# Kernel optimization log

Hardware: AMD Instinct MI355X
Metric: run time of the kernel (lower is better)

## Reference

```python
import jax, jax.numpy as jnp
import numpy as np

FP8_MAX = 448.0  # max representable magnitude of float8_e4m3fn


def _quantize_tensorwise(x):
    """Tensor-wise fp8 quantization. Returns (fp8 tensor, inverse_scale) where
    dequant = fp8.astype(f32) * inverse_scale (matches Fp8Quantization.quantize_tensorwise)."""
    amax = jnp.max(jnp.abs(x))
    inv_scale = jnp.maximum(amax / FP8_MAX, jnp.float32(1e-12))
    q = (x / inv_scale).astype(jnp.float8_e4m3fn)
    return q, inv_scale


def _fp8_mm(qa, qb, sa, sb):
    # scaled fp8 GEMM: accumulate in f32, apply product of per-tensor inverse scales
    return (qa.astype(jnp.float32) @ qb.astype(jnp.float32)) * (sa * sb)


def setup_inputs() -> dict:
    key = jax.random.key(0)
    k1, k2, k3 = jax.random.split(key, 3)
    x = jax.random.normal(k1, (4, 2048, 2048), dtype=jnp.float32)
    weight = jax.random.normal(k2, (2048, 2048), dtype=jnp.float32) * 0.02
    bias = jax.random.normal(k3, (2048,), dtype=jnp.float32) * 0.01
    return {"x": x, "weight": weight, "bias": bias}


def reference(x, weight, bias):
    # flatten leading dims: inputmat = input.view(-1, K)
    K = x.shape[-1]
    xm = x.reshape(-1, K)                      # [T, K]
    qx, sx = _quantize_tensorwise(xm)          # fp8 input + inverse scale
    qwt, swt = _quantize_tensorwise(weight.T)  # fp8 weight^T [K, N] + inverse scale
    out = _fp8_mm(qx, qwt, sx, swt) + bias     # [T, N]
    return out.reshape(*x.shape[:-1], -1)
```

## Files before the change

### kernel.cpp

```cpp
#include <hip/hip_runtime.h>
#include <stdint.h>

typedef float f32x4 __attribute__((ext_vector_type(4)));
typedef int   i32x4 __attribute__((ext_vector_type(4)));
typedef int   i32x8 __attribute__((ext_vector_type(8)));

__device__ __forceinline__ float amax4(float4 v) {
  return fmaxf(fmaxf(fabsf(v.x), fabsf(v.y)), fmaxf(fabsf(v.z), fabsf(v.w)));
}

__global__ __launch_bounds__(256) void amax2_kernel(
    const float* __restrict__ x, int nx4,
    const float* __restrict__ w, int nw4,
    int xblocks, int* __restrict__ out) {
  const float4* src;
  int n4, j0, stride, slot;
  if ((int)blockIdx.x < xblocks) {
    src = (const float4*)x; n4 = nx4; slot = 0;
    j0 = blockIdx.x * blockDim.x + threadIdx.x;
    stride = xblocks * blockDim.x;
  } else {
    src = (const float4*)w; n4 = nw4; slot = 1;
    j0 = (blockIdx.x - xblocks) * blockDim.x + threadIdx.x;
    stride = (gridDim.x - xblocks) * blockDim.x;
  }
  float m0 = 0.f, m1 = 0.f, m2 = 0.f, m3 = 0.f;
  int j = j0;
  for (; j + 3 * stride < n4; j += 4 * stride) {
    float4 v0 = src[j];
    float4 v1 = src[j + stride];
    float4 v2 = src[j + 2 * stride];
    float4 v3 = src[j + 3 * stride];
    m0 = fmaxf(m0, amax4(v0));
    m1 = fmaxf(m1, amax4(v1));
    m2 = fmaxf(m2, amax4(v2));
    m3 = fmaxf(m3, amax4(v3));
  }
  for (; j < n4; j += stride) m0 = fmaxf(m0, amax4(src[j]));
  float m = fmaxf(fmaxf(m0, m1), fmaxf(m2, m3));
#pragma unroll
  for (int off = 32; off; off >>= 1)
    m = fmaxf(m, __shfl_down(m, off, 64));
  __shared__ float red[4];
  const int lane = threadIdx.x & 63;
  const int wv = threadIdx.x >> 6;
  if (lane == 0) red[wv] = m;
  __syncthreads();
  if (threadIdx.x == 0) {
    m = fmaxf(fmaxf(red[0], red[1]), fmaxf(red[2], red[3]));
    atomicMax(out + slot, (int)__float_as_uint(m));
  }
}

__global__ __launch_bounds__(256) void quant2_kernel(
    const float* __restrict__ x, unsigned char* __restrict__ qx, int nx4,
    const float* __restrict__ w, unsigned char* __restrict__ qw, int nw4,
    int xblocks, const unsigned* __restrict__ amax2) {
  const float4* src;
  unsigned* dst;
  int n4, j0, stride;
  float amax;
  if ((int)blockIdx.x < xblocks) {
    src = (const float4*)x; dst = (unsigned*)qx; n4 = nx4;
    amax = __uint_as_float(amax2[0]);
    j0 = blockIdx.x * blockDim.x + threadIdx.x;
    stride = xblocks * blockDim.x;
  } else {
    src = (const float4*)w; dst = (unsigned*)qw; n4 = nw4;
    amax = __uint_as_float(amax2[1]);
    j0 = (blockIdx.x - xblocks) * blockDim.x + threadIdx.x;
    stride = (gridDim.x - xblocks) * blockDim.x;
  }
  const float inv_scale = fmaxf(amax / 448.0f, 1e-12f);
  int j = j0;
  for (; j + 3 * stride < n4; j += 4 * stride) {
    float4 v0 = src[j];
    float4 v1 = src[j + stride];
    float4 v2 = src[j + 2 * stride];
    float4 v3 = src[j + 3 * stride];
#pragma unroll
    for (int u = 0; u < 4; u++) {
      float4 v = (u == 0) ? v0 : (u == 1) ? v1 : (u == 2) ? v2 : v3;
      float a0 = v.x / inv_scale;
      float a1 = v.y / inv_scale;
      float a2 = v.z / inv_scale;
      float a3 = v.w / inv_scale;
      int p = 0;
      p = __builtin_amdgcn_cvt_pk_fp8_f32(a0, a1, p, false);
      p = __builtin_amdgcn_cvt_pk_fp8_f32(a2, a3, p, true);
      dst[j + u * stride] = (unsigned)p;
    }
  }
  for (; j < n4; j += stride) {
    float4 v = src[j];
    float a0 = v.x / inv_scale;
    float a1 = v.y / inv_scale;
    float a2 = v.z / inv_scale;
    float a3 = v.w / inv_scale;
    int p = 0;
    p = __builtin_amdgcn_cvt_pk_fp8_f32(a0, a1, p, false);
    p = __builtin_amdgcn_cvt_pk_fp8_f32(a2, a3, p, true);
    dst[j] = (unsigned)p;
  }
}

#define BM 128
#define BN 128
#define BK 128

__device__ __forceinline__ void load_lds16(const void* g, void* l) {
  __builtin_amdgcn_global_load_lds(
      (const __attribute__((address_space(1))) unsigned int*)g,
      (__attribute__((address_space(3))) unsigned int*)l, 16, 0, 0);
}

__global__ __launch_bounds__(256) void gemm_fp8_kernel(
    const unsigned char* __restrict__ Aq,
    const unsigned char* __restrict__ Bq,
    const float* __restrict__ bias,
    const unsigned* __restrict__ amax2,
    float* __restrict__ out,
    int T, int N, int K) {
  __shared__ __align__(16) unsigned char sA[BM * BK];
  __shared__ __align__(16) unsigned char sB[BN * BK];

  const int tid = threadIdx.x;
  const int lane = tid & 63;
  const int wave = tid >> 6;
  const int wm = (wave >> 1) * 64;
  const int wn = (wave & 1) * 64;
  const long m0 = (long)blockIdx.y * BM;
  const long n0 = (long)blockIdx.x * BN;

  f32x4 acc[4][4];
#pragma unroll
  for (int i = 0; i < 4; i++)
#pragma unroll
    for (int j = 0; j < 4; j++) acc[i][j] = (f32x4){0.f, 0.f, 0.f, 0.f};

  const int row_s = tid >> 3;
  const int c_s = tid & 7;
  const int scol = (c_s ^ (row_s & 7)) << 4;
  const int o = tid * 16;
  const unsigned char* aSrc[4];
  const unsigned char* bSrc[4];
#pragma unroll
  for (int r = 0; r < 4; r++) {
    aSrc[r] = Aq + (m0 + r * 32 + row_s) * (long)K + scol;
    bSrc[r] = Bq + (n0 + r * 32 + row_s) * (long)K + scol;
  }

  const int lm = lane & 15;
  const int q = lane >> 4;
  const int kc0 = q * 2;
  const int sxr = lm & 7;

  for (int k0 = 0; k0 < K; k0 += BK) {
#pragma unroll
    for (int r = 0; r < 4; r++) {
      load_lds16(aSrc[r] + k0, sA + r * 4096 + o);
      load_lds16(bSrc[r] + k0, sB + r * 4096 + o);
    }
    __syncthreads();

    i32x8 af[4], bf[4];
    const int c0 = (kc0 ^ sxr) << 4;
    const int c1 = ((kc0 + 1) ^ sxr) << 4;
#pragma unroll
    for (int mt = 0; mt < 4; mt++) {
      const unsigned char* p = sA + (wm + mt * 16 + lm) * BK;
      i32x4 lo = *(const i32x4*)(p + c0);
      i32x4 hi = *(const i32x4*)(p + c1);
      af[mt] = (i32x8){lo.x, lo.y, lo.z, lo.w, hi.x, hi.y, hi.z, hi.w};
    }
#pragma unroll
    for (int nt = 0; nt < 4; nt++) {
      const unsigned char* p = sB + (wn + nt * 16 + lm) * BK;
      i32x4 lo = *(const i32x4*)(p + c0);
      i32x4 hi = *(const i32x4*)(p + c1);
      bf[nt] = (i32x8){lo.x, lo.y, lo.z, lo.w, hi.x, hi.y, hi.z, hi.w};
    }
#pragma unroll
    for (int mt = 0; mt < 4; mt++)
#pragma unroll
      for (int nt = 0; nt < 4; nt++)
        acc[mt][nt] = __builtin_amdgcn_mfma_scale_f32_16x16x128_f8f6f4(
            af[mt], bf[nt], acc[mt][nt],
             0,  0,
             0, 0x7f7f7f7f,  0, 0x7f7f7f7f);
    __syncthreads();
  }

  const float sx = fmaxf(__uint_as_float(amax2[0]) / 448.0f, 1e-12f);
  const float sw = fmaxf(__uint_as_float(amax2[1]) / 448.0f, 1e-12f);
  const float scale = sx * sw;
  const int rbase = (lane >> 4) * 4;
#pragma unroll
  for (int mt = 0; mt < 4; mt++) {
#pragma unroll
    for (int r = 0; r < 4; r++) {
      const long row = m0 + wm + mt * 16 + rbase + r;
      float* orow = out + row * (long)N + n0 + wn;
#pragma unroll
      for (int nt = 0; nt < 4; nt++) {
        const int col = nt * 16 + lm;
        orow[col] = acc[mt][nt][r] * scale + bias[n0 + wn + col];
      }
    }
  }
}

extern "C" void kernel_launch(void* const* d_in, const int* in_sizes, int n_in,
                              void* d_out, int out_size, void* d_ws, size_t ws_size,
                              hipStream_t stream) {
  const float* x = (const float*)d_in[0];
  const float* w = (const float*)d_in[1];
  const float* bias = (const float*)d_in[2];
  float* out = (float*)d_out;

  const int N = in_sizes[2];
  const int K = in_sizes[1] / N;
  const int T = in_sizes[0] / K;

  unsigned* amax2 = (unsigned*)d_ws;
  unsigned char* qx = (unsigned char*)d_ws + 256;
  unsigned char* qw = qx + (size_t)T * K;

  const int XB = 2048;
  const int WB = 512;
  amax2_kernel<<<XB + WB, 256, 0, stream>>>(x, T * K / 4, w, N * K / 4, XB,
                                            (int*)amax2);
  quant2_kernel<<<XB + WB, 256, 0, stream>>>(x, qx, T * K / 4, w, qw, N * K / 4,
                                             XB, amax2);

  dim3 grid(N / BN, T / BM);
  gemm_fp8_kernel<<<grid, 256, 0, stream>>>(qx, qw, bias, amax2, out, T, N, K);
}
```

Before: 197.4 us.

## Use 32x32x64 fp8 MFMA with 256x128 GEMM tiles

Switches the GEMM from 16x16x128 scaled MFMA to 32x32x64 scaled MFMA and doubles the M tile to 256, so each wave computes a 128x64 sub-tile. Each LDS fragment is reused across more output, lowering LDS read and global load traffic per FLOP. It also hoists bias loads and sets launch bounds to request two blocks per CU. In exchange it uses 48KB of LDS and 128 accumulator registers per thread, which may reduce occupancy. The grid halves to 512 blocks.

```diff
diff --git a/kernel.cpp b/kernel.cpp
--- a/kernel.cpp
+++ b/kernel.cpp
@@ -1,7 +1,7 @@
 #include <hip/hip_runtime.h>
 #include <stdint.h>
 
-typedef float f32x4 __attribute__((ext_vector_type(4)));
+typedef float f32x16 __attribute__((ext_vector_type(16)));
 typedef int   i32x4 __attribute__((ext_vector_type(4)));
 typedef int   i32x8 __attribute__((ext_vector_type(8)));
 
@@ -104,7 +104,7 @@
   }
 }
 
-#define BM 128
+#define BM 256
 #define BN 128
 #define BK 128
 
@@ -114,7 +114,7 @@
       (__attribute__((address_space(3))) unsigned int*)l, 16, 0, 0);
 }
 
-__global__ __launch_bounds__(256) void gemm_fp8_kernel(
+__global__ __launch_bounds__(256, 2) void gemm_fp8_kernel(
     const unsigned char* __restrict__ Aq,
     const unsigned char* __restrict__ Bq,
     const float* __restrict__ bias,
@@ -127,85 +127,84 @@
   const int tid = threadIdx.x;
   const int lane = tid & 63;
   const int wave = tid >> 6;
-  const int wm = (wave >> 1) * 64;
+  const int wm = (wave >> 1) * 128;
   const int wn = (wave & 1) * 64;
   const long m0 = (long)blockIdx.y * BM;
   const long n0 = (long)blockIdx.x * BN;
 
-  f32x4 acc[4][4];
+  f32x16 acc[4][2];
 #pragma unroll
   for (int i = 0; i < 4; i++)
 #pragma unroll
-    for (int j = 0; j < 4; j++) acc[i][j] = (f32x4){0.f, 0.f, 0.f, 0.f};
+    for (int j = 0; j < 2; j++)
+#pragma unroll
+      for (int r = 0; r < 16; r++) acc[i][j][r] = 0.f;
 
   const int row_s = tid >> 3;
-  const int c_s = tid & 7;
-  const int scol = (c_s ^ (row_s & 7)) << 4;
+  const int scol = ((tid & 7) ^ (row_s & 7)) << 4;
   const int o = tid * 16;
-  const unsigned char* aSrc[4];
-  const unsigned char* bSrc[4];
-#pragma unroll
-  for (int r = 0; r < 4; r++) {
-    aSrc[r] = Aq + (m0 + r * 32 + row_s) * (long)K + scol;
-    bSrc[r] = Bq + (n0 + r * 32 + row_s) * (long)K + scol;
-  }
-
-  const int lm = lane & 15;
-  const int q = lane >> 4;
-  const int kc0 = q * 2;
-  const int sxr = lm & 7;
+  const unsigned char* aBase = Aq + (m0 + row_s) * (long)K + scol;
+  const unsigned char* bBase = Bq + (n0 + row_s) * (long)K + scol;
+
+  const int lr = lane & 31;
+  const int kh = lane >> 5;
+  const int swz = lr & 7;
 
   for (int k0 = 0; k0 < K; k0 += BK) {
 #pragma unroll
-    for (int r = 0; r < 4; r++) {
-      load_lds16(aSrc[r] + k0, sA + r * 4096 + o);
-      load_lds16(bSrc[r] + k0, sB + r * 4096 + o);
+    for (int r = 0; r < 8; r++)
+      load_lds16(aBase + (long)r * 32 * K + k0, sA + r * 4096 + o);
+#pragma unroll
+    for (int r = 0; r < 4; r++)
+      load_lds16(bBase + (long)r * 32 * K + k0, sB + r * 4096 + o);
+    __syncthreads();
+
+#pragma unroll
+    for (int s = 0; s < 2; s++) {
+      const int kc0 = s * 4 + kh * 2;
+      const int c0 = (kc0 ^ swz) << 4;
+      const int c1 = ((kc0 + 1) ^ swz) << 4;
+      i32x8 af[4], bf[2];
+#pragma unroll
+      for (int mt = 0; mt < 4; mt++) {
+        const unsigned char* p = sA + (wm + mt * 32 + lr) * BK;
+        i32x4 lo = *(const i32x4*)(p + c0);
+        i32x4 hi = *(const i32x4*)(p + c1);
+        af[mt] = (i32x8){lo.x, lo.y, lo.z, lo.w, hi.x, hi.y, hi.z, hi.w};
+      }
+#pragma unroll
+      for (int nt = 0; nt < 2; nt++) {
+        const unsigned char* p = sB + (wn + nt * 32 + lr) * BK;
+        i32x4 lo = *(const i32x4*)(p + c0);
+        i32x4 hi = *(const i32x4*)(p + c1);
+        bf[nt] = (i32x8){lo.x, lo.y, lo.z, lo.w, hi.x, hi.y, hi.z, hi.w};
+      }
+#pragma unroll
+      for (int mt = 0; mt < 4; mt++)
+#pragma unroll
+        for (int nt = 0; nt < 2; nt++)
+          acc[mt][nt] = __builtin_amdgcn_mfma_scale_f32_32x32x64_f8f6f4(
+              af[mt], bf[nt], acc[mt][nt],
+               0,  0,
+               0, 0x7f7f7f7f,  0, 0x7f7f7f7f);
     }
-    __syncthreads();
-
-    i32x8 af[4], bf[4];
-    const int c0 = (kc0 ^ sxr) << 4;
-    const int c1 = ((kc0 + 1) ^ sxr) << 4;
-#pragma unroll
-    for (int mt = 0; mt < 4; mt++) {
-      const unsigned char* p = sA + (wm + mt * 16 + lm) * BK;
-      i32x4 lo = *(const i32x4*)(p + c0);
-      i32x4 hi = *(const i32x4*)(p + c1);
-      af[mt] = (i32x8){lo.x, lo.y, lo.z, lo.w, hi.x, hi.y, hi.z, hi.w};
-    }
-#pragma unroll
-    for (int nt = 0; nt < 4; nt++) {
-      const unsigned char* p = sB + (wn + nt * 16 + lm) * BK;
-      i32x4 lo = *(const i32x4*)(p + c0);
-      i32x4 hi = *(const i32x4*)(p + c1);
-      bf[nt] = (i32x8){lo.x, lo.y, lo.z, lo.w, hi.x, hi.y, hi.z, hi.w};
-    }
-#pragma unroll
-    for (int mt = 0; mt < 4; mt++)
-#pragma unroll
-      for (int nt = 0; nt < 4; nt++)
-        acc[mt][nt] = __builtin_amdgcn_mfma_scale_f32_16x16x128_f8f6f4(
-            af[mt], bf[nt], acc[mt][nt],
-             0,  0,
-             0, 0x7f7f7f7f,  0, 0x7f7f7f7f);
     __syncthreads();
   }
 
   const float sx = fmaxf(__uint_as_float(amax2[0]) / 448.0f, 1e-12f);
   const float sw = fmaxf(__uint_as_float(amax2[1]) / 448.0f, 1e-12f);
   const float scale = sx * sw;
-  const int rbase = (lane >> 4) * 4;
+  const float bv0 = bias[n0 + wn + lr];
+  const float bv1 = bias[n0 + wn + 32 + lr];
 #pragma unroll
   for (int mt = 0; mt < 4; mt++) {
 #pragma unroll
-    for (int r = 0; r < 4; r++) {
-      const long row = m0 + wm + mt * 16 + rbase + r;
-      float* orow = out + row * (long)N + n0 + wn;
-#pragma unroll
-      for (int nt = 0; nt < 4; nt++) {
-        const int col = nt * 16 + lm;
-        orow[col] = acc[mt][nt][r] * scale + bias[n0 + wn + col];
-      }
+    for (int reg = 0; reg < 16; reg++) {
+      const long row =
+          m0 + wm + mt * 32 + (reg & 3) + 8 * (reg >> 2) + 4 * kh;
+      float* orow = out + row * (long)N + n0 + wn + lr;
+      orow[0] = acc[mt][0][reg] * scale + bv0;
+      orow[32] = acc[mt][1][reg] * scale + bv1;
     }
   }
 }
```

Measured after the change: 190.2 us. 3.6% less time.
